# Kernel tuning notes

Measured on AMD Instinct MI355X. Metric: run time of the kernel, lower is better.

## Reference

```python
import jax, jax.numpy as jnp
import numpy as np

N = 2048      # num nodes
F = 64        # in_channels
H = 16        # hidden_channels
O = 8         # out_channels


def setup_inputs() -> dict:
    key = jax.random.key(0)
    ks = jax.random.split(key, 16)
    s = 0.2  # small init scale
    inp = {
        "x": jax.random.normal(ks[0], (N, F), jnp.float32),
        "node_distances": jax.random.uniform(ks[1], (N, N), jnp.float32) * 5.0,
        "normalization": jax.random.uniform(ks[2], (N, N), jnp.float32) + 0.5,
        # per-feature f MLPs (1 -> H -> H -> O), stacked over features
        "fW1": jax.random.normal(ks[3], (F, H), jnp.float32) * s,
        "fb1": jnp.zeros((F, H), jnp.float32),
        "fW2": jax.random.normal(ks[4], (F, H, H), jnp.float32) * s,  # [F, out, in]
        "fb2": jnp.zeros((F, H), jnp.float32),
        "fW3": jax.random.normal(ks[5], (F, O, H), jnp.float32) * s,  # [F, out, in]
        "fb3": jnp.zeros((F, O), jnp.float32),
        # shared m MLP (1 -> H -> H -> 1), limited_m=True
        "mW1": jax.random.normal(ks[6], (H,), jnp.float32) * s,
        "mb1": jnp.zeros((H,), jnp.float32),
        "mW2": jax.random.normal(ks[7], (H, H), jnp.float32) * s,    # [out, in]
        "mb2": jnp.zeros((H,), jnp.float32),
        "mW3": jax.random.normal(ks[8], (H,), jnp.float32) * s,
        "mb3": jnp.zeros((), jnp.float32),
    }
    return inp


def reference(x, node_distances, normalization,
              fW1, fb1, fW2, fb2, fW3, fb3,
              mW1, mb1, mW2, mb2, mW3, mb3):
    # ---- per-feature f MLPs, vectorized over all nodes and features ----
    # x: [N, F] -> h: [N, F, H]
    h = jax.nn.relu(x[:, :, None] * fW1[None] + fb1[None])
    h = jax.nn.relu(jnp.einsum('nfh,fgh->nfg', h, fW2) + fb2[None])
    fx = jnp.einsum('nfh,foh->nfo', h, fW3) + fb3[None]        # [N, F, O]
    f_sums = fx.sum(axis=1)                                    # [N, O]

    # ---- m MLP applied elementwise to all pairwise distances ----
    d = node_distances                                         # [N, N]
    hm = jax.nn.relu(d[:, :, None] * mW1 + mb1)                # [N, N, H]
    hm = jax.nn.relu(jnp.einsum('ijh,gh->ijg', hm, mW2) + mb2)
    m_out = jnp.einsum('ijh,h->ij', hm, mW3) + mb3             # [N, N] (out dim 1)

    # normalize_m=True, m output dim == 1
    m_norm = m_out / normalization                             # [N, N]

    # pred[i] = sum_j m_norm[i, j] * f_sums[j]
    return m_norm @ f_sums                                     # [N, O]
```

## Files before the change

### kernel.cpp

```cpp
#include <hip/hip_runtime.h>

#define NN 2048
#define FF 64
#define HH 16
#define OO 8

#define BIGF  1e30f
#define BIGTH 1e29f
#define MAXBP 288
#define BPPAD 512
#define ABPAD 320

__device__ inline void l1_pattern(float c, const float* w1, const float* b1,
                                  float* a1, float* v1)
{
#pragma unroll
    for (int h = 0; h < HH; ++h) {
        const float arg = fmaf(w1[h], c, b1[h]);
        const bool act = arg > 0.f;
        a1[h] = act ? w1[h] : 0.f;
        v1[h] = act ? b1[h] : 0.f;
    }
}

__device__ inline void l2_arg(float c, int g,
                              const float* w1, const float* b1,
                              const float* w2, const float* b2,
                              float& A, float& B)
{
    float a1[HH], v1[HH];
    l1_pattern(c, w1, b1, a1, v1);
    float Aa = 0.f, Bb = b2[g];
#pragma unroll
    for (int h = 0; h < HH; ++h) {
        Aa = fmaf(w2[g * HH + h], a1[h], Aa);
        Bb = fmaf(w2[g * HH + h], v1[h], Bb);
    }
    A = Aa; B = Bb;
}

__device__ inline void pwl_coeffs(float c,
                                  const float* w1, const float* b1,
                                  const float* w2, const float* b2,
                                  const float* w3, float b3,
                                  float& alpha, float& beta)
{
    float a1[HH], v1[HH];
    l1_pattern(c, w1, b1, a1, v1);
    float al = 0.f, be = b3;
#pragma unroll
    for (int g = 0; g < HH; ++g) {
        float A = 0.f, B = b2[g];
#pragma unroll
        for (int h = 0; h < HH; ++h) {
            A = fmaf(w2[g * HH + h], a1[h], A);
            B = fmaf(w2[g * HH + h], v1[h], B);
        }
        const bool act = fmaf(A, c, B) > 0.f;
        al = fmaf(w3[g], act ? A : 0.f, al);
        be = fmaf(w3[g], act ? B : 0.f, be);
    }
    alpha = al; beta = be;
}

__device__ inline float seg_midpoint(float L, float R)
{
    float c;
    if (L <= -BIGTH && R >= BIGTH) c = 2.5f;
    else if (L <= -BIGTH)          c = R - 1.f;
    else if (R >= BIGTH)           c = L + 1.f;
    else                           c = 0.5f * (L + R);
    return fminf(fmaxf(c, -20.f), 20.f);
}

__global__ __launch_bounds__(512) void pwl_setup(
    const float* __restrict__ mW1, const float* __restrict__ mb1,
    const float* __restrict__ mW2, const float* __restrict__ mb2,
    const float* __restrict__ mW3, const float* __restrict__ mb3,
    float* __restrict__ bp_out, float* __restrict__ ab_out)
{
    __shared__ float w1[HH], b1[HH], w2[HH * HH], b2[HH], w3[HH];
    __shared__ float b3s;
    __shared__ float ends[18];
    __shared__ float cand[MAXBP];
    __shared__ float sorted[MAXBP];
    __shared__ float t16s[HH];
    const int tid = threadIdx.x;

    if (tid < HH) { w1[tid] = mW1[tid]; b1[tid] = mb1[tid]; b2[tid] = mb2[tid]; w3[tid] = mW3[tid]; }
    if (tid < HH * HH) w2[tid] = mW2[tid];
    if (tid == 0) b3s = mb3[0];
    __syncthreads();

    if (tid < HH) {
        const float w = w1[tid];
        const float t = -b1[tid] / w;
        cand[tid] = (w != 0.f && t > -10.f && t < 10.f) ? t : BIGF;
    }
    __syncthreads();
    if (tid < HH) {
        const float my = cand[tid];
        int r = 0;
        for (int k = 0; k < HH; ++k) {
            const float o = cand[k];
            r += (o < my) || (o == my && k < tid);
        }
        t16s[r] = my;
    }
    __syncthreads();
    if (tid == 0)  ends[0] = -BIGF;
    if (tid < HH)  ends[tid + 1] = t16s[tid];
    if (tid == 0)  ends[17] = BIGF;
    __syncthreads();

    if (tid < 17 * HH) {
        const int iv = tid >> 4;
        const int g  = tid & 15;
        const float L = ends[iv], R = ends[iv + 1];
        float x = BIGF;
        if (L < BIGTH) {
            const float c = seg_midpoint(L, R);
            float A, B;
            l2_arg(c, g, w1, b1, w2, b2, A, B);
            const float xx = -B / A;
            if (xx > L && xx < R && xx > -10.f && xx < 10.f) x = xx;
        }
        cand[HH + tid] = x;
    }
    __syncthreads();

    if (tid < MAXBP) {
        const float my = cand[tid];
        int r = 0;
        for (int k = 0; k < MAXBP; ++k) {
            const float o = cand[k];
            r += (o < my) || (o == my && k < tid);
        }
        sorted[r] = my;
    }
    __syncthreads();

    bp_out[tid] = (tid < MAXBP) ? sorted[tid] : BIGF;

    if (tid < ABPAD) {
        float al = 0.f, be = 0.f;
        if (tid <= MAXBP) {
            const float L = (tid == 0)     ? -BIGF : sorted[tid - 1];
            const float R = (tid < MAXBP)  ? sorted[tid] : BIGF;
            const float c = seg_midpoint(L, R);
            pwl_coeffs(c, w1, b1, w2, b2, w3, b3s, al, be);
        }
        ab_out[tid] = al;
        ab_out[ABPAD + tid] = be;
    }
}

__global__ __launch_bounds__(256) void fnet_kernel(
    const float* __restrict__ x,
    const float* __restrict__ fW1, const float* __restrict__ fb1,
    const float* __restrict__ fW2, const float* __restrict__ fb2,
    const float* __restrict__ fW3, const float* __restrict__ fb3,
    float* __restrict__ part)
{
    __shared__ float sw1[HH], sb1[HH], sw2[HH * HH], sb2[HH], sw3[OO * HH], sb3[OO];
    const int f = blockIdx.x;
    const int tid = threadIdx.x;

    if (tid < HH) {
        sw1[tid] = fW1[f * HH + tid];
        sb1[tid] = fb1[f * HH + tid];
        sb2[tid] = fb2[f * HH + tid];
    }
    if (tid < HH * HH) sw2[tid] = fW2[f * HH * HH + tid];
    if (tid < OO * HH) sw3[tid] = fW3[f * OO * HH + tid];
    if (tid < OO)      sb3[tid] = fb3[f * OO + tid];
    __syncthreads();

    const int n = blockIdx.y * 256 + tid;
    const float xv = x[n * FF + f];

    float h1[HH];
#pragma unroll
    for (int h = 0; h < HH; ++h)
        h1[h] = fmaxf(xv * sw1[h] + sb1[h], 0.f);

    float h2[HH];
#pragma unroll
    for (int g = 0; g < HH; ++g) {
        float a = sb2[g];
#pragma unroll
        for (int h = 0; h < HH; ++h) a += sw2[g * HH + h] * h1[h];
        h2[g] = fmaxf(a, 0.f);
    }

#pragma unroll
    for (int o = 0; o < OO; ++o) {
        float a = sb3[o];
#pragma unroll
        for (int h = 0; h < HH; ++h) a += sw3[o * HH + h] * h2[h];
        part[(n * FF + f) * OO + o] = a;
    }
}

__global__ __launch_bounds__(64) void fsum_reduce(
    const float* __restrict__ part, float* __restrict__ f_sums)
{
    const int n = blockIdx.x;
    const int f = threadIdx.x;
    const float4* p = reinterpret_cast<const float4*>(part + (n * FF + f) * OO);
    float4 a = p[0];
    float4 b = p[1];
#pragma unroll
    for (int off = 32; off > 0; off >>= 1) {
        a.x += __shfl_down(a.x, off, 64);
        a.y += __shfl_down(a.y, off, 64);
        a.z += __shfl_down(a.z, off, 64);
        a.w += __shfl_down(a.w, off, 64);
        b.x += __shfl_down(b.x, off, 64);
        b.y += __shfl_down(b.y, off, 64);
        b.z += __shfl_down(b.z, off, 64);
        b.w += __shfl_down(b.w, off, 64);
    }
    if (f == 0) {
        float4* q = reinterpret_cast<float4*>(f_sums + n * OO);
        q[0] = a;
        q[1] = b;
    }
}

__global__ __launch_bounds__(256) void mnet_pwl(
    const float* __restrict__ d, const float* __restrict__ norm,
    const float* __restrict__ f_sums,
    const float* __restrict__ bp_g, const float* __restrict__ ab_g,
    float* __restrict__ out)
{
    __shared__ float sbp[BPPAD];
    __shared__ float sal[ABPAD], sbe[ABPAD];
    __shared__ float red[4][OO];
    const int i = blockIdx.x;
    const int tid = threadIdx.x;

    for (int k = tid; k < BPPAD; k += 256) sbp[k] = bp_g[k];
    for (int k = tid; k < ABPAD; k += 256) { sal[k] = ab_g[k]; sbe[k] = ab_g[ABPAD + k]; }
    __syncthreads();

    float acc[OO];
#pragma unroll
    for (int o = 0; o < OO; ++o) acc[o] = 0.f;

    const float* drow = d + (size_t)i * NN;
    const float* nrow = norm + (size_t)i * NN;

#pragma unroll
    for (int ch = 0; ch < 2; ++ch) {
        const int j0 = ch * 1024 + (tid << 2);
        const float4 dv4 = *reinterpret_cast<const float4*>(drow + j0);
        const float4 nv4 = *reinterpret_cast<const float4*>(nrow + j0);
        const float dvs[4] = {dv4.x, dv4.y, dv4.z, dv4.w};
        const float nvs[4] = {nv4.x, nv4.y, nv4.z, nv4.w};
#pragma unroll
        for (int e = 0; e < 4; ++e) {
            const float dv = dvs[e];
            int lo = 0;
#pragma unroll
            for (int st = 256; st >= 1; st >>= 1)
                lo += (sbp[lo + st - 1] <= dv) ? st : 0;
            const float mn = fmaf(sal[lo], dv, sbe[lo]) / nvs[e];
            const float4 f0 = *reinterpret_cast<const float4*>(f_sums + (j0 + e) * OO);
            const float4 f1 = *reinterpret_cast<const float4*>(f_sums + (j0 + e) * OO + 4);
            acc[0] = fmaf(mn, f0.x, acc[0]);
            acc[1] = fmaf(mn, f0.y, acc[1]);
            acc[2] = fmaf(mn, f0.z, acc[2]);
            acc[3] = fmaf(mn, f0.w, acc[3]);
            acc[4] = fmaf(mn, f1.x, acc[4]);
            acc[5] = fmaf(mn, f1.y, acc[5]);
            acc[6] = fmaf(mn, f1.z, acc[6]);
            acc[7] = fmaf(mn, f1.w, acc[7]);
        }
    }

#pragma unroll
    for (int off = 32; off > 0; off >>= 1) {
#pragma unroll
        for (int o = 0; o < OO; ++o) acc[o] += __shfl_down(acc[o], off, 64);
    }
    const int wave = tid >> 6;
    const int lane = tid & 63;
    if (lane == 0) {
#pragma unroll
        for (int o = 0; o < OO; ++o) red[wave][o] = acc[o];
    }
    __syncthreads();
    if (tid == 0) {
#pragma unroll
        for (int o = 0; o < OO; ++o)
            out[i * OO + o] = red[0][o] + red[1][o] + red[2][o] + red[3][o];
    }
}

extern "C" void kernel_launch(void* const* d_in, const int* in_sizes, int n_in,
                              void* d_out, int out_size, void* d_ws, size_t ws_size,
                              hipStream_t stream)
{
    const float* x   = (const float*)d_in[0];
    const float* nd  = (const float*)d_in[1];
    const float* nm  = (const float*)d_in[2];
    const float* fW1 = (const float*)d_in[3];
    const float* fb1 = (const float*)d_in[4];
    const float* fW2 = (const float*)d_in[5];
    const float* fb2 = (const float*)d_in[6];
    const float* fW3 = (const float*)d_in[7];
    const float* fb3 = (const float*)d_in[8];
    const float* mW1 = (const float*)d_in[9];
    const float* mb1 = (const float*)d_in[10];
    const float* mW2 = (const float*)d_in[11];
    const float* mb2 = (const float*)d_in[12];
    const float* mW3 = (const float*)d_in[13];
    const float* mb3 = (const float*)d_in[14];
    float* out = (float*)d_out;

    float* part   = (float*)d_ws;
    float* f_sums = part + (size_t)NN * FF * OO;
    float* bp     = f_sums + (size_t)NN * OO;
    float* ab     = bp + BPPAD;

    pwl_setup<<<1, 512, 0, stream>>>(mW1, mb1, mW2, mb2, mW3, mb3, bp, ab);
    fnet_kernel<<<dim3(FF, NN / 256), 256, 0, stream>>>(
        x, fW1, fb1, fW2, fb2, fW3, fb3, part);
    fsum_reduce<<<NN, 64, 0, stream>>>(part, f_sums);
    mnet_pwl<<<NN, 256, 0, stream>>>(nd, nm, f_sums, bp, ab, out);
}
```

Before: 51.37 us.

## Replace breakpoint binary search with uniform-grid cell lookup and merge setup kernels

```diff
diff --git a/kernel.cpp b/kernel.cpp
--- a/kernel.cpp
+++ b/kernel.cpp
@@ -10,6 +10,17 @@
 #define MAXBP 288
 #define BPPAD 512
 #define ABPAD 320
+#define GCELL 1024
+
+__device__ inline int cell_of(float d)
+{
+    int k = (int)floorf(fmaf(d, 32.f, 512.f));
+    return min(max(k, 0), GCELL - 1);
+}
+__device__ inline int keycell(float v)
+{
+    return (v > BIGTH) ? GCELL : cell_of(v);
+}
 
 __device__ inline void l1_pattern(float c, const float* w1, const float* b1,
                                   float* a1, float* v1)
@@ -73,23 +84,73 @@
     return fminf(fmaxf(c, -20.f), 20.f);
 }
 
-__global__ __launch_bounds__(512) void pwl_setup(
+__global__ __launch_bounds__(512) void setup_kernel(
+    const float* __restrict__ x,
+    const float* __restrict__ fW1, const float* __restrict__ fb1,
+    const float* __restrict__ fW2, const float* __restrict__ fb2,
+    const float* __restrict__ fW3, const float* __restrict__ fb3,
     const float* __restrict__ mW1, const float* __restrict__ mb1,
     const float* __restrict__ mW2, const float* __restrict__ mb2,
     const float* __restrict__ mW3, const float* __restrict__ mb3,
-    float* __restrict__ bp_out, float* __restrict__ ab_out)
-{
+    float* __restrict__ part,
+    float* __restrict__ bp_out, float* __restrict__ ab_out,
+    float* __restrict__ cell4_out, float* __restrict__ cellb_out)
+{
+    const int tid = threadIdx.x;
+
+    if (blockIdx.x < 256) {
+        __shared__ float sw1[HH], sb1[HH], sw2[HH * HH], sb2[HH], sw3[OO * HH], sb3[OO];
+        const int f = blockIdx.x & 63;
+
+        if (tid < HH) {
+            sw1[tid] = fW1[f * HH + tid];
+            sb1[tid] = fb1[f * HH + tid];
+            sb2[tid] = fb2[f * HH + tid];
+        }
+        if (tid < HH * HH) sw2[tid] = fW2[f * HH * HH + tid];
+        if (tid < OO * HH) sw3[tid] = fW3[f * OO * HH + tid];
+        if (tid < OO)      sb3[tid] = fb3[f * OO + tid];
+        __syncthreads();
+
+        const int n = (blockIdx.x >> 6) * 512 + tid;
+        const float xv = x[n * FF + f];
+
+        float h1[HH];
+#pragma unroll
+        for (int h = 0; h < HH; ++h)
+            h1[h] = fmaxf(fmaf(xv, sw1[h], sb1[h]), 0.f);
+
+        float h2[HH];
+#pragma unroll
+        for (int g = 0; g < HH; ++g) {
+            float a = sb2[g];
+#pragma unroll
+            for (int h = 0; h < HH; ++h) a = fmaf(sw2[g * HH + h], h1[h], a);
+            h2[g] = fmaxf(a, 0.f);
+        }
+
+#pragma unroll
+        for (int o = 0; o < OO; ++o) {
+            float a = sb3[o];
+#pragma unroll
+            for (int h = 0; h < HH; ++h) a = fmaf(sw3[o * HH + h], h2[h], a);
+            part[(n * FF + f) * OO + o] = a;
+        }
+        return;
+    }
+
     __shared__ float w1[HH], b1[HH], w2[HH * HH], b2[HH], w3[HH];
     __shared__ float b3s;
     __shared__ float ends[18];
     __shared__ float cand[MAXBP];
-    __shared__ float sorted[MAXBP];
+    __shared__ float sorted[BPPAD];
     __shared__ float t16s[HH];
-    const int tid = threadIdx.x;
+    __shared__ float sal[ABPAD], sbe[ABPAD];
 
     if (tid < HH) { w1[tid] = mW1[tid]; b1[tid] = mb1[tid]; b2[tid] = mb2[tid]; w3[tid] = mW3[tid]; }
     if (tid < HH * HH) w2[tid] = mW2[tid];
     if (tid == 0) b3s = mb3[0];
+    sorted[tid] = BIGF;
     __syncthreads();
 
     if (tid < HH) {
@@ -117,15 +178,15 @@
         const int iv = tid >> 4;
         const int g  = tid & 15;
         const float L = ends[iv], R = ends[iv + 1];
-        float x = BIGF;
+        float xx = BIGF;
         if (L < BIGTH) {
             const float c = seg_midpoint(L, R);
             float A, B;
             l2_arg(c, g, w1, b1, w2, b2, A, B);
-            const float xx = -B / A;
-            if (xx > L && xx < R && xx > -10.f && xx < 10.f) x = xx;
-        }
-        cand[HH + tid] = x;
+            const float t = -B / A;
+            if (t > L && t < R && t > -10.f && t < 10.f) xx = t;
+        }
+        cand[HH + tid] = xx;
     }
     __syncthreads();
 
@@ -140,73 +201,56 @@
     }
     __syncthreads();
 
-    bp_out[tid] = (tid < MAXBP) ? sorted[tid] : BIGF;
+    bp_out[tid] = sorted[tid];
 
     if (tid < ABPAD) {
         float al = 0.f, be = 0.f;
         if (tid <= MAXBP) {
-            const float L = (tid == 0)     ? -BIGF : sorted[tid - 1];
-            const float R = (tid < MAXBP)  ? sorted[tid] : BIGF;
+            const float L = (tid == 0)    ? -BIGF : sorted[tid - 1];
+            const float R = (tid < MAXBP) ? sorted[tid] : BIGF;
             const float c = seg_midpoint(L, R);
             pwl_coeffs(c, w1, b1, w2, b2, w3, b3s, al, be);
         }
+        sal[tid] = al; sbe[tid] = be;
         ab_out[tid] = al;
         ab_out[ABPAD + tid] = be;
     }
-}
-
-__global__ __launch_bounds__(256) void fnet_kernel(
-    const float* __restrict__ x,
-    const float* __restrict__ fW1, const float* __restrict__ fb1,
-    const float* __restrict__ fW2, const float* __restrict__ fb2,
-    const float* __restrict__ fW3, const float* __restrict__ fb3,
-    float* __restrict__ part)
-{
-    __shared__ float sw1[HH], sb1[HH], sw2[HH * HH], sb2[HH], sw3[OO * HH], sb3[OO];
-    const int f = blockIdx.x;
-    const int tid = threadIdx.x;
-
-    if (tid < HH) {
-        sw1[tid] = fW1[f * HH + tid];
-        sb1[tid] = fb1[f * HH + tid];
-        sb2[tid] = fb2[f * HH + tid];
-    }
-    if (tid < HH * HH) sw2[tid] = fW2[f * HH * HH + tid];
-    if (tid < OO * HH) sw3[tid] = fW3[f * OO * HH + tid];
-    if (tid < OO)      sb3[tid] = fb3[f * OO + tid];
-    __syncthreads();
-
-    const int n = blockIdx.y * 256 + tid;
-    const float xv = x[n * FF + f];
-
-    float h1[HH];
-#pragma unroll
-    for (int h = 0; h < HH; ++h)
-        h1[h] = fmaxf(xv * sw1[h] + sb1[h], 0.f);
-
-    float h2[HH];
-#pragma unroll
-    for (int g = 0; g < HH; ++g) {
-        float a = sb2[g];
-#pragma unroll
-        for (int h = 0; h < HH; ++h) a += sw2[g * HH + h] * h1[h];
-        h2[g] = fmaxf(a, 0.f);
-    }
-
-#pragma unroll
-    for (int o = 0; o < OO; ++o) {
-        float a = sb3[o];
-#pragma unroll
-        for (int h = 0; h < HH; ++h) a += sw3[o * HH + h] * h2[h];
-        part[(n * FF + f) * OO + o] = a;
-    }
-}
-
-__global__ __launch_bounds__(64) void fsum_reduce(
+    __syncthreads();
+
+    for (int k = tid; k < GCELL; k += 512) {
+        int base = 0, nxt = 0;
+#pragma unroll
+        for (int st = 256; st >= 1; st >>= 1) {
+            base += (keycell(sorted[base + st - 1]) < k)     ? st : 0;
+            nxt  += (keycell(sorted[nxt  + st - 1]) < k + 1) ? st : 0;
+        }
+        const int cnt = nxt - base;
+        float4 r; float bk;
+        if (cnt == 0) {
+            r.x = sal[base]; r.y = sbe[base]; r.z = r.x; r.w = r.y;
+            bk = -BIGF;
+        } else {
+            const float bmin = sorted[base];
+            const float bmax = sorted[nxt - 1];
+            if (bmin == bmax) {
+                r.x = sal[base];       r.y = sbe[base];
+                r.z = sal[base + cnt]; r.w = sbe[base + cnt];
+                bk = bmin;
+            } else {
+                r.x = r.y = r.z = r.w = 0.f;
+                bk = __int_as_float(0x7fc00000);
+            }
+        }
+        reinterpret_cast<float4*>(cell4_out)[k] = r;
+        cellb_out[k] = bk;
+    }
+}
+
+__global__ __launch_bounds__(256) void fsum_reduce(
     const float* __restrict__ part, float* __restrict__ f_sums)
 {
-    const int n = blockIdx.x;
-    const int f = threadIdx.x;
+    const int n = blockIdx.x * 4 + (threadIdx.x >> 6);
+    const int f = threadIdx.x & 63;
     const float4* p = reinterpret_cast<const float4*>(part + (n * FF + f) * OO);
     float4 a = p[0];
     float4 b = p[1];
@@ -228,32 +272,40 @@
     }
 }
 
-__global__ __launch_bounds__(256) void mnet_pwl(
+__global__ __launch_bounds__(256) void mnet_kernel(
     const float* __restrict__ d, const float* __restrict__ norm,
     const float* __restrict__ f_sums,
     const float* __restrict__ bp_g, const float* __restrict__ ab_g,
+    const float* __restrict__ cell4_g, const float* __restrict__ cellb_g,
     float* __restrict__ out)
 {
-    __shared__ float sbp[BPPAD];
-    __shared__ float sal[ABPAD], sbe[ABPAD];
-    __shared__ float red[4][OO];
-    const int i = blockIdx.x;
+    __shared__ float4 sc4[GCELL];
+    __shared__ float  scb[GCELL];
+    __shared__ float  sbp[BPPAD], sal[ABPAD], sbe[ABPAD];
     const int tid = threadIdx.x;
 
+    for (int k = tid; k < GCELL; k += 256) {
+        sc4[k] = reinterpret_cast<const float4*>(cell4_g)[k];
+        scb[k] = cellb_g[k];
+    }
     for (int k = tid; k < BPPAD; k += 256) sbp[k] = bp_g[k];
     for (int k = tid; k < ABPAD; k += 256) { sal[k] = ab_g[k]; sbe[k] = ab_g[ABPAD + k]; }
     __syncthreads();
 
-    float acc[OO];
-#pragma unroll
-    for (int o = 0; o < OO; ++o) acc[o] = 0.f;
+    const int w = tid >> 6;
+    const int lane = tid & 63;
+    const int i = blockIdx.x * 4 + w;
 
     const float* drow = d + (size_t)i * NN;
     const float* nrow = norm + (size_t)i * NN;
 
-#pragma unroll
-    for (int ch = 0; ch < 2; ++ch) {
-        const int j0 = ch * 1024 + (tid << 2);
+    float acc[OO];
+#pragma unroll
+    for (int o = 0; o < OO; ++o) acc[o] = 0.f;
+
+#pragma unroll
+    for (int it = 0; it < NN / 256; ++it) {
+        const int j0 = (it * 64 + lane) * 4;
         const float4 dv4 = *reinterpret_cast<const float4*>(drow + j0);
         const float4 nv4 = *reinterpret_cast<const float4*>(nrow + j0);
         const float dvs[4] = {dv4.x, dv4.y, dv4.z, dv4.w};
@@ -261,11 +313,19 @@
 #pragma unroll
         for (int e = 0; e < 4; ++e) {
             const float dv = dvs[e];
-            int lo = 0;
-#pragma unroll
-            for (int st = 256; st >= 1; st >>= 1)
-                lo += (sbp[lo + st - 1] <= dv) ? st : 0;
-            const float mn = fmaf(sal[lo], dv, sbe[lo]) / nvs[e];
+            const int k = cell_of(dv);
+            const float4 r = sc4[k];
+            const float bk = scb[k];
+            float al = (dv < bk) ? r.x : r.z;
+            float be = (dv < bk) ? r.y : r.w;
+            if (bk != bk) {
+                int lo = 0;
+#pragma unroll
+                for (int st = 256; st >= 1; st >>= 1)
+                    lo += (sbp[lo + st - 1] <= dv) ? st : 0;
+                al = sal[lo]; be = sbe[lo];
+            }
+            const float mn = fmaf(al, dv, be) * __builtin_amdgcn_rcpf(nvs[e]);
             const float4 f0 = *reinterpret_cast<const float4*>(f_sums + (j0 + e) * OO);
             const float4 f1 = *reinterpret_cast<const float4*>(f_sums + (j0 + e) * OO + 4);
             acc[0] = fmaf(mn, f0.x, acc[0]);
@@ -284,17 +344,9 @@
 #pragma unroll
         for (int o = 0; o < OO; ++o) acc[o] += __shfl_down(acc[o], off, 64);
     }
-    const int wave = tid >> 6;
-    const int lane = tid & 63;
     if (lane == 0) {
 #pragma unroll
-        for (int o = 0; o < OO; ++o) red[wave][o] = acc[o];
-    }
-    __syncthreads();
-    if (tid == 0) {
-#pragma unroll
-        for (int o = 0; o < OO; ++o)
-            out[i * OO + o] = red[0][o] + red[1][o] + red[2][o] + red[3][o];
+        for (int o = 0; o < OO; ++o) out[i * OO + o] = acc[o];
     }
 }
 
@@ -323,10 +375,13 @@
     float* f_sums = part + (size_t)NN * FF * OO;
     float* bp     = f_sums + (size_t)NN * OO;
     float* ab     = bp + BPPAD;
-
-    pwl_setup<<<1, 512, 0, stream>>>(mW1, mb1, mW2, mb2, mW3, mb3, bp, ab);
-    fnet_kernel<<<dim3(FF, NN / 256), 256, 0, stream>>>(
-        x, fW1, fb1, fW2, fb2, fW3, fb3, part);
-    fsum_reduce<<<NN, 64, 0, stream>>>(part, f_sums);
-    mnet_pwl<<<NN, 256, 0, stream>>>(nd, nm, f_sums, bp, ab, out);
-}
+    float* cell4  = ab + 2 * ABPAD;
+    float* cellb  = cell4 + 4 * GCELL;
+
+    setup_kernel<<<257, 512, 0, stream>>>(
+        x, fW1, fb1, fW2, fb2, fW3, fb3,
+        mW1, mb1, mW2, mb2, mW3, mb3,
+        part, bp, ab, cell4, cellb);
+    fsum_reduce<<<512, 256, 0, stream>>>(part, f_sums);
+    mnet_kernel<<<512, 256, 0, stream>>>(nd, nm, f_sums, bp, ab, cell4, cellb, out);
+}
```

Measured after the change: 47.76 us. 7.0% less time.
